# Kernel tuning notes

Measured on AMD Instinct MI355X. Metric: run time of the kernel, lower is better.

Reference implementation:

```python
import jax, jax.numpy as jnp
import numpy as np

B, XL, YL = 4, 128, 1024
D, H, L, DFF = 512, 8, 3, 2048
PV, AV, OV = 512, 1025, 1025
MASK_ID = 1024
EOS = 1024
DUR_W = 1.0
NEG = -1e9  # finite large-negative instead of -inf: keeps fully-padded rows NaN-free
HD = D // H
S = XL + 1 + YL


def sinusoid(n, d):
    pos = jnp.arange(n, dtype=jnp.float32)[:, None]
    div = jnp.exp(jnp.arange(0, d, 2, dtype=jnp.float32) * (-np.log(10000.0) / d))
    pe = jnp.zeros((n, d), dtype=jnp.float32)
    pe = pe.at[:, 0::2].set(jnp.sin(pos * div))
    pe = pe.at[:, 1::2].set(jnp.cos(pos * div))
    return pe


def layer_norm(x, g, b, eps=1e-5):
    mu = x.mean(-1, keepdims=True)
    var = ((x - mu) ** 2).mean(-1, keepdims=True)
    return (x - mu) * jax.lax.rsqrt(var + eps) * g + b


def setup_inputs():
    k = jax.random.split(jax.random.key(0), 32)
    x = jax.random.randint(k[0], (B, XL), 0, PV)
    x1_lens = jax.random.randint(k[1], (B,), 20, 60)
    x2_lens = jax.random.randint(k[2], (B,), 20, 60)
    y = jax.random.randint(k[3], (B, YL), 0, AV - 2)
    y1_lens = jax.random.randint(k[4], (B,), 100, 400)
    y2_lens = jax.random.randint(k[5], (B,), 300, 600)
    y_lens = y1_lens + 1 + y2_lens
    idx = jnp.arange(YL)[None, :]
    valid = (idx >= y1_lens[:, None] + 1) & (idx < y_lens[:, None] - 1)
    bern = jax.random.uniform(k[6], (B, YL)) < 0.3  # mask_ratio = mid(min,max)
    ym = bern & valid
    need = (~ym.any(1)) & valid.any(1)
    first = jnp.argmax(valid, axis=1)
    y_mask = ym | (need[:, None] & (idx == first[:, None]))
    emo_feature = jax.random.normal(k[7], (B, 768), dtype=jnp.float32)

    def n(kk, shape, s=0.02):
        return s * jax.random.normal(kk, shape, dtype=jnp.float32)

    inp = dict(x=x, x1_lens=x1_lens, x2_lens=x2_lens, y=y, y1_lens=y1_lens,
               y2_lens=y2_lens, y_mask=y_mask, emo_feature=emo_feature)
    inp['text_emb'] = n(k[8], (PV, D))
    inp['audio_emb'] = n(k[9], (AV, D))
    inp['type_emb'] = n(k[10], (3, D))
    inp['emo_W'] = n(k[11], (D, 768))
    inp['emo_b'] = jnp.zeros((D,), jnp.float32)
    inp['alpha_text'] = jnp.float32(1.0)
    inp['alpha_audio'] = jnp.float32(1.0)
    inp['Wqkv'] = n(k[12], (L, 3 * D, D))
    inp['bqkv'] = jnp.zeros((L, 3 * D), jnp.float32)
    inp['Wo'] = n(k[13], (L, D, D))
    inp['bo'] = jnp.zeros((L, D), jnp.float32)
    inp['ln1_g'] = jnp.ones((L, D), jnp.float32)
    inp['ln1_b'] = jnp.zeros((L, D), jnp.float32)
    inp['ln2_g'] = jnp.ones((L, D), jnp.float32)
    inp['ln2_b'] = jnp.zeros((L, D), jnp.float32)
    inp['W1'] = n(k[14], (L, DFF, D))
    inp['b1'] = jnp.zeros((L, DFF), jnp.float32)
    inp['W2'] = n(k[15], (L, D, DFF))
    inp['b2'] = jnp.zeros((L, D), jnp.float32)
    inp['predict_W'] = n(k[16], (OV, D))
    inp['dW1'] = n(k[17], (D // 2, D))
    inp['db1'] = jnp.zeros((D // 2,), jnp.float32)
    inp['dW2'] = n(k[18], (D // 4, D // 2))
    inp['db2'] = jnp.zeros((D // 4,), jnp.float32)
    inp['dW3'] = n(k[19], (1, D // 4))
    inp['db3'] = jnp.zeros((1,), jnp.float32)
    return inp


def build_attn_bias(x1_lens, x2_lens, y1_lens, y2_lens, y_mask):
    x_lens = x1_lens + 1 + x2_lens
    y_lens = y1_lens + 1 + y2_lens
    cS = jnp.arange(S)[None, :]  # [1,S] key columns
    # --- x rows ---
    rx = jnp.arange(XL)[None, :]
    is_x1 = rx < x1_lens[:, None]                                   # [B,XL]
    allow_x1 = cS < x1_lens[:, None]                                # [B,S]
    allow_x2 = (cS >= x1_lens[:, None]) & (cS < x_lens[:, None])
    x_allow = jnp.where(is_x1[:, :, None], allow_x1[:, None, :], allow_x2[:, None, :])
    # --- emo row: attends only to itself (col XL) ---
    emo_allow = jnp.broadcast_to((cS == XL)[:, None, :], (B, 1, S))
    # --- y rows ---
    ry = jnp.arange(YL)[None, :]
    is_y1 = ry < y1_lens[:, None]
    is_cls = ry == y1_lens[:, None]
    is_y2 = (ry > y1_lens[:, None]) & (ry < y_lens[:, None])
    allow_y1 = (cS < x1_lens[:, None]) | ((cS > XL) & (cS <= XL + y1_lens[:, None]))
    allow_cls = (cS < x_lens[:, None]) | (cS == XL) | ((cS > XL) & (cS <= XL + y1_lens[:, None] + 1))
    allow_y2 = (cS < x_lens[:, None]) | (cS == XL) | ((cS > XL) & (cS <= XL + y_lens[:, None]))
    ymask_full = jnp.zeros((B, S), bool).at[:, XL + 1:].set(y_mask)
    allow_y2 = allow_y2 & (~ymask_full)                             # masked tokens invisible
    y_allow = jnp.where(is_y1[:, :, None], allow_y1[:, None, :],
               jnp.where(is_cls[:, :, None], allow_cls[:, None, :],
                jnp.where(is_y2[:, :, None], allow_y2[:, None, :], False)))
    block = ~jnp.concatenate([x_allow, emo_allow, y_allow], axis=1)  # True = blocked
    return jnp.where(block, jnp.float32(NEG), jnp.float32(0.0))[:, None]  # [B,1,S,S]


def encoder_forward(h, bias, Wqkv, bqkv, Wo, bo, ln1_g, ln1_b, ln2_g, ln2_b, W1, b1, W2, b2):
    scale = 1.0 / np.sqrt(HD)
    for l in range(L):
        qkv = h @ Wqkv[l].T + bqkv[l]                               # [B,S,3D]
        q, k, v = jnp.split(qkv, 3, axis=-1)
        q = q.reshape(B, S, H, HD).transpose(0, 2, 1, 3)
        k = k.reshape(B, S, H, HD).transpose(0, 2, 1, 3)
        v = v.reshape(B, S, H, HD).transpose(0, 2, 1, 3)
        scores = jnp.einsum('bhqd,bhkd->bhqk', q, k) * scale + bias
        a = jax.nn.softmax(scores, axis=-1)
        o = jnp.einsum('bhqk,bhkd->bhqd', a, v).transpose(0, 2, 1, 3).reshape(B, S, D)
        o = o @ Wo[l].T + bo[l]
        h = layer_norm(h + o, ln1_g[l], ln1_b[l])                   # post-norm
        ff = jax.nn.relu(h @ W1[l].T + b1[l]) @ W2[l].T + b2[l]
        h = layer_norm(h + ff, ln2_g[l], ln2_b[l])
    return h


def reference(x, x1_lens, x2_lens, y, y1_lens, y2_lens, y_mask, emo_feature,
              text_emb, audio_emb, type_emb, emo_W, emo_b, alpha_text, alpha_audio,
              Wqkv, bqkv, Wo, bo, ln1_g, ln1_b, ln2_g, ln2_b, W1, b1, W2, b2,
              predict_W, dW1, db1, dW2, db2, dW3, db3):
    y_target = y
    x_emb = text_emb[x] + type_emb[0]
    x_pos = x_emb + alpha_text * sinusoid(XL, D)
    emo = emo_feature @ emo_W.T + emo_b + type_emb[1]
    y_in = jnp.where(y_mask, MASK_ID, y)
    y_emb = audio_emb[y_in] + type_emb[2]
    y_pos = y_emb + alpha_audio * sinusoid(YL, D)
    h_input = jnp.concatenate([x_pos, emo[:, None, :], y_pos], axis=1)  # [B,S,D]
    bias = build_attn_bias(x1_lens, x2_lens, y1_lens, y2_lens, y_mask)
    enc = encoder_forward(h_input, bias, Wqkv, bqkv, Wo, bo,
                          ln1_g, ln1_b, ln2_g, ln2_b, W1, b1, W2, b2)
    # duration loss on CLS hidden at prompt_lens = XL + 1 + y1_lens
    cls_hidden = enc[jnp.arange(B), XL + 1 + y1_lens]
    h1 = jax.nn.relu(cls_hidden @ dW1.T + db1)
    h2 = jax.nn.relu(h1 @ dW2.T + db2)
    pred_dur = (h2 @ dW3.T + db3)[:, 0]
    tgt_dur = y2_lens.astype(jnp.float32) / x2_lens.astype(jnp.float32)
    e = pred_dur - tgt_dur
    dur_loss = jnp.mean(jnp.where(jnp.abs(e) <= 1.0, 0.5 * e * e, jnp.abs(e) - 0.5))
    # token CE over masked positions (mean over masked tokens)
    logits = enc[:, XL + 1:] @ predict_W.T                          # [B,YL,OV]
    logp = jax.nn.log_softmax(logits, axis=-1)
    ce = -jnp.take_along_axis(logp, y_target[..., None], axis=-1)[..., 0]
    m = y_mask.astype(jnp.float32)
    token_loss = jnp.sum(ce * m) / jnp.sum(m)
    # top-3 accuracy ignoring EOS
    top3 = jax.lax.top_k(logits, 3)[1]
    correct = jnp.any(top3 == y_target[..., None], axis=-1)
    inc = (y_mask & (y_target != EOS)).astype(jnp.float32)
    acc = jnp.sum(correct.astype(jnp.float32) * inc) / jnp.maximum(jnp.sum(inc), 1.0)
    total_loss = token_loss + DUR_W * dur_loss
    return total_loss, acc
```

## Files before the change

kernel.cpp:

```cpp
#include <hip/hip_runtime.h>
#include <hip/hip_bf16.h>
#include <math.h>

#define BATCH 4
#define XL 128
#define YL 1024
#define DMODEL 512
#define NH 8
#define NLAYER 3
#define DFF 2048
#define MASK_ID 1024
#define EOS_TOK 1024
#define HD 64
#define SEQ 1153
#define OV 1025
#define NEGBIG (-1e9f)
#define QBLK 128
#define CCAP 2432

typedef unsigned short u16;
typedef short short8 __attribute__((ext_vector_type(8)));
typedef float f32x4 __attribute__((ext_vector_type(4)));

__device__ __forceinline__ u16 f2bf(float f) {
    union { float f; unsigned u; } v; v.f = f;
    unsigned r = v.u + 0x7fffu + ((v.u >> 16) & 1u);
    return (u16)(r >> 16);
}
__device__ __forceinline__ float bf2f(u16 b) {
    union { unsigned u; float f; } v; v.u = ((unsigned)b) << 16;
    return v.f;
}

__global__ __launch_bounds__(256) void cvt5_kernel(
    const float* __restrict__ s0, u16* __restrict__ d0, int n0,
    const float* __restrict__ s1, u16* __restrict__ d1, int n1,
    const float* __restrict__ s2, u16* __restrict__ d2, int n2,
    const float* __restrict__ s3, u16* __restrict__ d3, int n3,
    const float* __restrict__ s4, u16* __restrict__ d4, int n4)
{
    int c0 = n0, c1 = c0 + n1, c2 = c1 + n2, c3 = c2 + n3, c4 = c3 + n4;
    for (int i = blockIdx.x * 256 + threadIdx.x; i < c4; i += gridDim.x * 256) {
        const float* s; u16* d; int j;
        if (i < c0)      { s = s0; d = d0; j = i; }
        else if (i < c1) { s = s1; d = d1; j = i - c0; }
        else if (i < c2) { s = s2; d = d2; j = i - c1; }
        else if (i < c3) { s = s3; d = d3; j = i - c2; }
        else             { s = s4; d = d4; j = i - c3; }
        float4 v = ((const float4*)s)[j];
        ushort4 o;
        o.x = f2bf(v.x); o.y = f2bf(v.y); o.z = f2bf(v.z); o.w = f2bf(v.w);
        ((ushort4*)d)[j] = o;
    }
}

__global__ __launch_bounds__(256) void emo_kernel(
    const float* __restrict__ emo_feature, const float* __restrict__ emo_W,
    const float* __restrict__ emo_b, const float* __restrict__ type_emb,
    float* __restrict__ hbuf, u16* __restrict__ hbuf_bf)
{
    int b = blockIdx.x >> 3, c = blockIdx.x & 7;
    int t = threadIdx.x;
    int osub = t >> 2, ln = t & 3;
    int d = c * 64 + osub;
    const float* f = emo_feature + b * 768 + ln * 192;
    const float* w = emo_W + (size_t)d * 768 + ln * 192;
    float acc = 0.f;
    #pragma unroll 4
    for (int k = 0; k < 192; ++k) acc = fmaf(f[k], w[k], acc);
    acc += __shfl_xor(acc, 1);
    acc += __shfl_xor(acc, 2);
    if (ln == 0) {
        float v = acc + emo_b[d] + type_emb[DMODEL + d];
        hbuf[(size_t)(b * SEQ + XL) * DMODEL + d] = v;
        hbuf_bf[(size_t)(b * SEQ + XL) * DMODEL + d] = f2bf(v);
    }
}

__global__ __launch_bounds__(256) void build_h_kernel(
    const int* __restrict__ x, const int* __restrict__ y, const int* __restrict__ y_mask,
    const float* __restrict__ text_emb, const float* __restrict__ audio_emb,
    const float* __restrict__ type_emb,
    const float* __restrict__ alpha_text, const float* __restrict__ alpha_audio,
    float* __restrict__ hbuf, u16* __restrict__ hbuf_bf)
{
    int row = blockIdx.x * 4 + (threadIdx.x >> 6);
    int l = threadIdx.x & 63;
    int b = row / SEQ, s = row % SEQ;
    if (s == XL) return;
    int d0 = l * 8;

    const float* emb; const float* te; float alpha; int pos;
    if (s < XL) {
        int tok = x[b * XL + s];
        emb = text_emb + (size_t)tok * DMODEL;
        te = type_emb; alpha = alpha_text[0]; pos = s;
    } else {
        int r = s - XL - 1;
        int tok = y_mask[b * YL + r] ? MASK_ID : y[b * YL + r];
        emb = audio_emb + (size_t)tok * DMODEL;
        te = type_emb + 2 * DMODEL; alpha = alpha_audio[0]; pos = r;
    }

    float4 e0 = *(const float4*)(emb + d0);
    float4 e1 = *(const float4*)(emb + d0 + 4);
    float4 t0 = *(const float4*)(te + d0);
    float4 t1 = *(const float4*)(te + d0 + 4);
    float v[8] = {e0.x + t0.x, e0.y + t0.y, e0.z + t0.z, e0.w + t0.w,
                  e1.x + t1.x, e1.y + t1.y, e1.z + t1.z, e1.w + t1.w};
    float fp = (float)pos;
    #pragma unroll
    for (int p = 0; p < 4; ++p) {
        int d = d0 + 2 * p;
        float div = __expf((float)d * (-9.210340371976184f / (float)DMODEL));
        float sn, cs;
        __sincosf(fp * div, &sn, &cs);
        v[2 * p]     += alpha * sn;
        v[2 * p + 1] += alpha * cs;
    }

    float* hp = hbuf + (size_t)row * DMODEL + d0;
    *(float4*)hp       = make_float4(v[0], v[1], v[2], v[3]);
    *(float4*)(hp + 4) = make_float4(v[4], v[5], v[6], v[7]);
    short8 sv;
    #pragma unroll
    for (int e = 0; e < 8; ++e) sv[e] = (short)f2bf(v[e]);
    *(short8*)(hbuf_bf + (size_t)row * DMODEL + d0) = sv;
}

__global__ __launch_bounds__(256) void gemm_bf16_kernel(
    const u16* __restrict__ A, const u16* __restrict__ Bw,
    const float* __restrict__ bias,
    float* __restrict__ Cf, u16* __restrict__ Cb,
    int M, int N, int K, int relu)
{
    __shared__ u16 As[128 * 32];
    __shared__ u16 Bs[128 * 32];
    int tid = threadIdx.x;
    int w = tid >> 6, l = tid & 63;
    int m0 = blockIdx.y * 128, n0 = blockIdx.x * 128;
    int wm = (w >> 1) * 64, wn = (w & 1) * 64;

    f32x4 acc[4][4];
    #pragma unroll
    for (int i = 0; i < 4; ++i)
        #pragma unroll
        for (int j = 0; j < 4; ++j) acc[i][j] = (f32x4){0.f, 0.f, 0.f, 0.f};

    int srow0 = (w << 5) + (l >> 2);
    int skp = (l & 3) << 3;

    for (int k0 = 0; k0 < K; k0 += 32) {
        #pragma unroll
        for (int c = 0; c < 2; ++c) {
            int row = srow0 + c * 16;
            int am = m0 + row; if (am >= M) am = M - 1;
            int bn = n0 + row; if (bn >= N) bn = N - 1;
            __builtin_amdgcn_global_load_lds(
                (const __attribute__((address_space(1))) void*)(A + (size_t)am * K + k0 + skp),
                (__attribute__((address_space(3))) void*)(As + ((w * 2 + c) << 9)), 16, 0, 0);
            __builtin_amdgcn_global_load_lds(
                (const __attribute__((address_space(1))) void*)(Bw + (size_t)bn * K + k0 + skp),
                (__attribute__((address_space(3))) void*)(Bs + ((w * 2 + c) << 9)), 16, 0, 0);
        }
        __syncthreads();
        short8 af[4], bfr[4];
        #pragma unroll
        for (int i = 0; i < 4; ++i) {
            af[i]  = *(const short8*)(As + (wm + i * 16 + (l & 15)) * 32 + ((l >> 4) << 3));
            bfr[i] = *(const short8*)(Bs + (wn + i * 16 + (l & 15)) * 32 + ((l >> 4) << 3));
        }
        #pragma unroll
        for (int i = 0; i < 4; ++i)
            #pragma unroll
            for (int j = 0; j < 4; ++j)
                acc[i][j] = __builtin_amdgcn_mfma_f32_16x16x32_bf16(af[i], bfr[j], acc[i][j], 0, 0, 0);
        __syncthreads();
    }

    #pragma unroll
    for (int i = 0; i < 4; ++i) {
        #pragma unroll
        for (int j = 0; j < 4; ++j) {
            #pragma unroll
            for (int jj = 0; jj < 4; ++jj) {
                int row = m0 + wm + i * 16 + ((l >> 4) << 2) + jj;
                int col = n0 + wn + j * 16 + (l & 15);
                if (row < M && col < N) {
                    float v = acc[i][j][jj];
                    if (bias) v += bias[col];
                    if (relu) v = fmaxf(v, 0.f);
                    if (Cf) Cf[(size_t)row * N + col] = v;
                    if (Cb) Cb[(size_t)row * N + col] = f2bf(v);
                }
            }
        }
    }
}

__global__ __launch_bounds__(256) void gemm_bf16_splitk_kernel(
    const u16* __restrict__ A, const u16* __restrict__ Bw,
    float* __restrict__ P0, float* __restrict__ P1, float* __restrict__ P2,
    int M, int N, int K, int klen)
{
    __shared__ u16 As[128 * 32];
    __shared__ u16 Bs[128 * 32];
    int tid = threadIdx.x;
    int w = tid >> 6, l = tid & 63;
    int z = blockIdx.z;
    float* Cp = (z == 0) ? P0 : (z == 1) ? P1 : P2;
    int kbeg = z * klen;
    int kend = min(kbeg + klen, K);
    int m0 = blockIdx.y * 128, n0 = blockIdx.x * 128;
    int wm = (w >> 1) * 64, wn = (w & 1) * 64;

    f32x4 acc[4][4];
    #pragma unroll
    for (int i = 0; i < 4; ++i)
        #pragma unroll
        for (int j = 0; j < 4; ++j) acc[i][j] = (f32x4){0.f, 0.f, 0.f, 0.f};

    int srow0 = (w << 5) + (l >> 2);
    int skp = (l & 3) << 3;

    for (int k0 = kbeg; k0 < kend; k0 += 32) {
        #pragma unroll
        for (int c = 0; c < 2; ++c) {
            int row = srow0 + c * 16;
            int am = m0 + row; if (am >= M) am = M - 1;
            int bn = n0 + row; if (bn >= N) bn = N - 1;
            __builtin_amdgcn_global_load_lds(
                (const __attribute__((address_space(1))) void*)(A + (size_t)am * K + k0 + skp),
                (__attribute__((address_space(3))) void*)(As + ((w * 2 + c) << 9)), 16, 0, 0);
            __builtin_amdgcn_global_load_lds(
                (const __attribute__((address_space(1))) void*)(Bw + (size_t)bn * K + k0 + skp),
                (__attribute__((address_space(3))) void*)(Bs + ((w * 2 + c) << 9)), 16, 0, 0);
        }
        __syncthreads();
        short8 af[4], bfr[4];
        #pragma unroll
        for (int i = 0; i < 4; ++i) {
            af[i]  = *(const short8*)(As + (wm + i * 16 + (l & 15)) * 32 + ((l >> 4) << 3));
            bfr[i] = *(const short8*)(Bs + (wn + i * 16 + (l & 15)) * 32 + ((l >> 4) << 3));
        }
        #pragma unroll
        for (int i = 0; i < 4; ++i)
            #pragma unroll
            for (int j = 0; j < 4; ++j)
                acc[i][j] = __builtin_amdgcn_mfma_f32_16x16x32_bf16(af[i], bfr[j], acc[i][j], 0, 0, 0);
        __syncthreads();
    }

    #pragma unroll
    for (int i = 0; i < 4; ++i) {
        #pragma unroll
        for (int j = 0; j < 4; ++j) {
            #pragma unroll
            for (int jj = 0; jj < 4; ++jj) {
                int row = m0 + wm + i * 16 + ((l >> 4) << 2) + jj;
                int col = n0 + wn + j * 16 + (l & 15);
                if (row < M && col < N)
                    Cp[(size_t)row * N + col] = acc[i][j][jj];
            }
        }
    }
}

__global__ __launch_bounds__(256) void gemm_bf16_splitk_dynm_kernel(
    const u16* __restrict__ A, const u16* __restrict__ Bw,
    const int* __restrict__ Mp,
    float* __restrict__ P0, float* __restrict__ P1,
    int N, int K, int klen)
{
    int M = *Mp;
    int m0 = blockIdx.y * 128;
    if (m0 >= M) return;
    __shared__ u16 As[128 * 32];
    __shared__ u16 Bs[128 * 32];
    int tid = threadIdx.x;
    int w = tid >> 6, l = tid & 63;
    int z = blockIdx.z;
    float* Cp = (z == 0) ? P0 : P1;
    int kbeg = z * klen;
    int kend = min(kbeg + klen, K);
    int n0 = blockIdx.x * 128;
    int wm = (w >> 1) * 64, wn = (w & 1) * 64;

    f32x4 acc[4][4];
    #pragma unroll
    for (int i = 0; i < 4; ++i)
        #pragma unroll
        for (int j = 0; j < 4; ++j) acc[i][j] = (f32x4){0.f, 0.f, 0.f, 0.f};

    int srow0 = (w << 5) + (l >> 2);
    int skp = (l & 3) << 3;

    for (int k0 = kbeg; k0 < kend; k0 += 32) {
        #pragma unroll
        for (int c = 0; c < 2; ++c) {
            int row = srow0 + c * 16;
            int am = m0 + row; if (am >= M) am = M - 1;
            int bn = n0 + row; if (bn >= N) bn = N - 1;
            __builtin_amdgcn_global_load_lds(
                (const __attribute__((address_space(1))) void*)(A + (size_t)am * K + k0 + skp),
                (__attribute__((address_space(3))) void*)(As + ((w * 2 + c) << 9)), 16, 0, 0);
            __builtin_amdgcn_global_load_lds(
                (const __attribute__((address_space(1))) void*)(Bw + (size_t)bn * K + k0 + skp),
                (__attribute__((address_space(3))) void*)(Bs + ((w * 2 + c) << 9)), 16, 0, 0);
        }
        __syncthreads();
        short8 af[4], bfr[4];
        #pragma unroll
        for (int i = 0; i < 4; ++i) {
            af[i]  = *(const short8*)(As + (wm + i * 16 + (l & 15)) * 32 + ((l >> 4) << 3));
            bfr[i] = *(const short8*)(Bs + (wn + i * 16 + (l & 15)) * 32 + ((l >> 4) << 3));
        }
        #pragma unroll
        for (int i = 0; i < 4; ++i)
            #pragma unroll
            for (int j = 0; j < 4; ++j)
                acc[i][j] = __builtin_amdgcn_mfma_f32_16x16x32_bf16(af[i], bfr[j], acc[i][j], 0, 0, 0);
        __syncthreads();
    }

    #pragma unroll
    for (int i = 0; i < 4; ++i) {
        #pragma unroll
        for (int j = 0; j < 4; ++j) {
            #pragma unroll
            for (int jj = 0; jj < 4; ++jj) {
                int row = m0 + wm + i * 16 + ((l >> 4) << 2) + jj;
                int col = n0 + wn + j * 16 + (l & 15);
                if (row < M && col < N)
                    Cp[(size_t)row * N + col] = acc[i][j][jj];
            }
        }
    }
}

__global__ __launch_bounds__(256) void attn_mfma_kernel(
    const u16* __restrict__ qkv,
    const int* __restrict__ x1_lens, const int* __restrict__ x2_lens,
    const int* __restrict__ y1_lens, const int* __restrict__ y2_lens,
    const int* __restrict__ y_mask,
    u16* __restrict__ obuf)
{
    __shared__ u16 Ks[64 * 64];
    __shared__ u16 Vt[64 * 64];
    __shared__ u16 Ps[4][32 * 64];
    __shared__ unsigned char Am[1216];

    int tid = threadIdx.x;
    int w = tid >> 6, l = tid & 63;
    int bh = blockIdx.y;
    int b = bh >> 3, h = bh & 7;
    int q0 = blockIdx.x * QBLK;

    int x1 = x1_lens[b], xlen = x1 + 1 + x2_lens[b];
    int y1 = y1_lens[b], ylen = y1 + 1 + y2_lens[b];

    int kmax = -1;
    if (q0 < XL) kmax = max(kmax, xlen - 1);
    if (XL >= q0 && XL < q0 + QBLK) kmax = max(kmax, XL);
    {
        int ry0 = max(0, q0 - XL - 1);
        int ry1 = min(YL - 1, q0 + QBLK - 2 - XL);
        if (ry0 <= ry1) {
            if (ry0 <= y1 - 1) kmax = max(kmax, XL + y1);
            if (y1 >= ry0 && y1 <= ry1) kmax = max(kmax, XL + y1 + 1);
            int a = max(ry0, y1 + 1), bb = min(ry1, ylen - 1);
            if (a <= bb) kmax = max(kmax, XL + ylen);
        }
    }
    if (kmax < 0) return;
    int NKT = (kmax >> 6) + 1;

    for (int c = tid; c < 1216; c += 256) {
        unsigned v = 0;
        if (c < SEQ) {
            int ym = 0;
            if (c > XL) ym = y_mask[b * YL + c - XL - 1];
            bool a2c = (c == XL);
            bool ygt = (c > XL);
            bool aT0 = (c < x1);
            bool aT1 = (c >= x1) && (c < xlen);
            bool aT3 = aT0 || (ygt && c <= XL + y1);
            bool aT4 = (c < xlen) || a2c || (ygt && c <= XL + y1 + 1);
            bool aT5 = (((c < xlen) || a2c || (ygt && c <= XL + ylen)) && !ym);
            v = (aT0 ? 1u : 0u) | (aT1 ? 2u : 0u) | (a2c ? 4u : 0u) |
                (aT3 ? 8u : 0u) | (aT4 ? 16u : 0u) | (aT5 ? 32u : 0u);
        }
        Am[c] = (unsigned char)v;
    }

    short8 qf[2][2];
    #pragma unroll
    for (int qh = 0; qh < 2; ++qh) {
        int qr = q0 + w * 32 + qh * 16 + (l & 15);
        const u16* qp = qkv + (size_t)(b * SEQ + qr) * 1536 + h * 64 + ((l >> 4) << 3);
        #pragma unroll
        for (int kb = 0; kb < 2; ++kb) {
            short8 raw = *(const short8*)(qp + kb * 32);
            short8 s8;
            #pragma unroll
            for (int e = 0; e < 8; ++e)
                s8[e] = (short)f2bf(bf2f((u16)raw[e]) * 0.125f);
            qf[qh][kb] = s8;
        }
    }

    int rt[2][4];
    #pragma unroll
    for (int qh = 0; qh < 2; ++qh)
        #pragma unroll
        for (int j = 0; j < 4; ++j) {
            int qrj = q0 + w * 32 + qh * 16 + ((l >> 4) << 2) + j;
            int t;
            if (qrj < XL) t = (qrj < x1) ? 0 : 1;
            else if (qrj == XL) t = 2;
            else {
                int ry = qrj - XL - 1;
                t = (ry < y1) ? 3 : (ry == y1) ? 4 : (ry < ylen) ? 5 : 7;
            }
            rt[qh][j] = t;
        }

    f32x4 oacc[2][4];
    #pragma unroll
    for (int qh = 0; qh < 2; ++qh)
        #pragma unroll
        for (int db = 0; db < 4; ++db) oacc[qh][db] = (f32x4){0.f, 0.f, 0.f, 0.f};
    float mrun[2][4], lrun[2][4];
    #pragma unroll
    for (int qh = 0; qh < 2; ++qh)
        #pragma unroll
        for (int j = 0; j < 4; ++j) { mrun[qh][j] = -INFINITY; lrun[qh][j] = 0.f; }
    u16* Psw = &Ps[w][0];

    for (int kt = 0; kt < NKT; ++kt) {
        __syncthreads();
        {
            int r = tid >> 2, d0k = (tid & 3) << 4;
            int krc = min(kt * 64 + r, SEQ - 1);
            const u16* kp = qkv + (size_t)(b * SEQ + krc) * 1536 + 512 + h * 64 + d0k;
            short8 ka = *(const short8*)kp;
            short8 kb8 = *(const short8*)(kp + 8);
            int ksw = (r & 7) << 3;
            *(short8*)&Ks[r * 64 + (d0k ^ ksw)] = ka;
            *(short8*)&Ks[r * 64 + ((d0k + 8) ^ ksw)] = kb8;
        }
        {
            int rp = tid >> 3, o = tid & 7;
            int d0v = o * 8;
            int k0r = min(kt * 64 + 2 * rp, SEQ - 1);
            int k1r = min(kt * 64 + 2 * rp + 1, SEQ - 1);
            const u16* v0p = qkv + (size_t)(b * SEQ + k0r) * 1536 + 1024 + h * 64 + d0v;
            const u16* v1p = qkv + (size_t)(b * SEQ + k1r) * 1536 + 1024 + h * 64 + d0v;
            short8 va = *(const short8*)v0p;
            short8 vb = *(const short8*)v1p;
            #pragma unroll
            for (int e = 0; e < 8; ++e) {
                int d = d0v + e;
                unsigned val = (unsigned)(u16)va[e] | ((unsigned)(u16)vb[e] << 16);
                *(unsigned*)&Vt[d * 64 + ((2 * rp) ^ ((d & 7) << 3))] = val;
            }
        }
        __syncthreads();

        unsigned amv[4];
        #pragma unroll
        for (int cb = 0; cb < 4; ++cb)
            amv[cb] = Am[kt * 64 + cb * 16 + (l & 15)];

        f32x4 sc[2][4];
        #pragma unroll
        for (int cb = 0; cb < 4; ++cb) {
            int krw = cb * 16 + (l & 15);
            int ksw = (krw & 7) << 3;
            short8 k0 = *(const short8*)&Ks[krw * 64 + ((((l >> 4) << 3)) ^ ksw)];
            short8 k1 = *(const short8*)&Ks[krw * 64 + ((32 + ((l >> 4) << 3)) ^ ksw)];
            #pragma unroll
            for (int qh = 0; qh < 2; ++qh) {
                f32x4 z = (f32x4){0.f, 0.f, 0.f, 0.f};
                z = __builtin_amdgcn_mfma_f32_16x16x32_bf16(qf[qh][0], k0, z, 0, 0, 0);
                sc[qh][cb] = __builtin_amdgcn_mfma_f32_16x16x32_bf16(qf[qh][1], k1, z, 0, 0, 0);
            }
        }

        #pragma unroll
        for (int qh = 0; qh < 2; ++qh) {
            #pragma unroll
            for (int j = 0; j < 4; ++j) {
                int rtj = rt[qh][j];
                float s0 = ((amv[0] >> rtj) & 1u) ? sc[qh][0][j] : NEGBIG;
                float s1 = ((amv[1] >> rtj) & 1u) ? sc[qh][1][j] : NEGBIG;
                float s2 = ((amv[2] >> rtj) & 1u) ? sc[qh][2][j] : NEGBIG;
                float s3 = ((amv[3] >> rtj) & 1u) ? sc[qh][3][j] : NEGBIG;
                float tmax = fmaxf(fmaxf(s0, s1), fmaxf(s2, s3));
                tmax = fmaxf(tmax, __shfl_xor(tmax, 1));
                tmax = fmaxf(tmax, __shfl_xor(tmax, 2));
                tmax = fmaxf(tmax, __shfl_xor(tmax, 4));
                tmax = fmaxf(tmax, __shfl_xor(tmax, 8));
                float newm = fmaxf(mrun[qh][j], tmax);
                float corr = __expf(mrun[qh][j] - newm);
                float p0 = __expf(s0 - newm);
                float p1 = __expf(s1 - newm);
                float p2 = __expf(s2 - newm);
                float p3 = __expf(s3 - newm);
                float ps = p0 + p1 + p2 + p3;
                ps += __shfl_xor(ps, 1); ps += __shfl_xor(ps, 2);
                ps += __shfl_xor(ps, 4); ps += __shfl_xor(ps, 8);
                lrun[qh][j] = lrun[qh][j] * corr + ps;
                mrun[qh][j] = newm;
                #pragma unroll
                for (int db = 0; db < 4; ++db) oacc[qh][db][j] *= corr;
                int lr = qh * 16 + ((l >> 4) << 2) + j;
                int sw = (lr & 7) << 3;
                Psw[lr * 64 + ((0  + (l & 15)) ^ sw)] = f2bf(p0);
                Psw[lr * 64 + ((16 + (l & 15)) ^ sw)] = f2bf(p1);
                Psw[lr * 64 + ((32 + (l & 15)) ^ sw)] = f2bf(p2);
                Psw[lr * 64 + ((48 + (l & 15)) ^ sw)] = f2bf(p3);
            }
        }

        short8 pf[2][2];
        #pragma unroll
        for (int qh = 0; qh < 2; ++qh) {
            int pr = qh * 16 + (l & 15);
            int sw = (pr & 7) << 3;
            pf[qh][0] = *(const short8*)&Psw[pr * 64 + ((((l >> 4) << 3)) ^ sw)];
            pf[qh][1] = *(const short8*)&Psw[pr * 64 + ((32 + ((l >> 4) << 3)) ^ sw)];
        }
        #pragma unroll
        for (int db = 0; db < 4; ++db) {
            int vr = db * 16 + (l & 15);
            int vsw = (vr & 7) << 3;
            short8 v0 = *(const short8*)&Vt[vr * 64 + ((((l >> 4) << 3)) ^ vsw)];
            short8 v1 = *(const short8*)&Vt[vr * 64 + ((32 + ((l >> 4) << 3)) ^ vsw)];
            #pragma unroll
            for (int qh = 0; qh < 2; ++qh) {
                oacc[qh][db] = __builtin_amdgcn_mfma_f32_16x16x32_bf16(pf[qh][0], v0, oacc[qh][db], 0, 0, 0);
                oacc[qh][db] = __builtin_amdgcn_mfma_f32_16x16x32_bf16(pf[qh][1], v1, oacc[qh][db], 0, 0, 0);
            }
        }
    }

    #pragma unroll
    for (int qh = 0; qh < 2; ++qh) {
        float rl[4];
        #pragma unroll
        for (int j = 0; j < 4; ++j) rl[j] = 1.f / lrun[qh][j];
        #pragma unroll
        for (int db = 0; db < 4; ++db) {
            #pragma unroll
            for (int j = 0; j < 4; ++j) {
                int qrj = q0 + w * 32 + qh * 16 + ((l >> 4) << 2) + j;
                obuf[(size_t)(b * SEQ + qrj) * DMODEL + h * 64 + db * 16 + (l & 15)] =
                    f2bf(oacc[qh][db][j] * rl[j]);
            }
        }
    }
}

__global__ __launch_bounds__(256) void add_ln_kernel(
    float* __restrict__ hbuf, u16* __restrict__ hbuf_bf,
    const float* __restrict__ p0, const float* __restrict__ p1,
    const float* __restrict__ p2, const float* __restrict__ bias,
    const float* __restrict__ g, const float* __restrict__ beta)
{
    int row = blockIdx.x * 4 + (threadIdx.x >> 6);
    int l = threadIdx.x & 63;
    int d0 = l * 8;
    size_t off = (size_t)row * DMODEL + d0;
    float* hp = hbuf + off;
    float4 a0 = *(const float4*)hp, a1 = *(const float4*)(hp + 4);
    float4 q0 = *(const float4*)(p0 + off), q1 = *(const float4*)(p0 + off + 4);
    float v[8] = {a0.x + q0.x, a0.y + q0.y, a0.z + q0.z, a0.w + q0.w,
                  a1.x + q1.x, a1.y + q1.y, a1.z + q1.z, a1.w + q1.w};
    if (p1) {
        float4 r0 = *(const float4*)(p1 + off), r1 = *(const float4*)(p1 + off + 4);
        v[0] += r0.x; v[1] += r0.y; v[2] += r0.z; v[3] += r0.w;
        v[4] += r1.x; v[5] += r1.y; v[6] += r1.z; v[7] += r1.w;
    }
    if (p2) {
        float4 r0 = *(const float4*)(p2 + off), r1 = *(const float4*)(p2 + off + 4);
        v[0] += r0.x; v[1] += r0.y; v[2] += r0.z; v[3] += r0.w;
        v[4] += r1.x; v[5] += r1.y; v[6] += r1.z; v[7] += r1.w;
    }
    {
        float4 b0 = *(const float4*)(bias + d0), b1 = *(const float4*)(bias + d0 + 4);
        v[0] += b0.x; v[1] += b0.y; v[2] += b0.z; v[3] += b0.w;
        v[4] += b1.x; v[5] += b1.y; v[6] += b1.z; v[7] += b1.w;
    }
    float s = 0.f;
    #pragma unroll
    for (int e = 0; e < 8; ++e) s += v[e];
    #pragma unroll
    for (int off2 = 32; off2 > 0; off2 >>= 1) s += __shfl_xor(s, off2);
    float mu = s * (1.f / DMODEL);
    float sq = 0.f;
    #pragma unroll
    for (int e = 0; e < 8; ++e) { v[e] -= mu; sq += v[e] * v[e]; }
    #pragma unroll
    for (int off2 = 32; off2 > 0; off2 >>= 1) sq += __shfl_xor(sq, off2);
    float inv = 1.f / sqrtf(sq * (1.f / DMODEL) + 1e-5f);
    float4 g0 = *(const float4*)(g + d0), g1 = *(const float4*)(g + d0 + 4);
    float4 be0 = *(const float4*)(beta + d0), be1 = *(const float4*)(beta + d0 + 4);
    float o[8];
    o[0] = v[0] * inv * g0.x + be0.x; o[1] = v[1] * inv * g0.y + be0.y;
    o[2] = v[2] * inv * g0.z + be0.z; o[3] = v[3] * inv * g0.w + be0.w;
    o[4] = v[4] * inv * g1.x + be1.x; o[5] = v[5] * inv * g1.y + be1.y;
    o[6] = v[6] * inv * g1.z + be1.z; o[7] = v[7] * inv * g1.w + be1.w;
    *(float4*)hp       = make_float4(o[0], o[1], o[2], o[3]);
    *(float4*)(hp + 4) = make_float4(o[4], o[5], o[6], o[7]);
    short8 sv;
    #pragma unroll
    for (int e = 0; e < 8; ++e) sv[e] = (short)f2bf(o[e]);
    *(short8*)(hbuf_bf + off) = sv;
}

__global__ __launch_bounds__(256) void init_accum_kernel(float* accum) {
    if (threadIdx.x < 8) accum[threadIdx.x] = 0.f;
}

__global__ __launch_bounds__(256) void compact_kernel(
    const int* __restrict__ y_mask, int* __restrict__ cnt, int* __restrict__ cmap)
{
    int i = blockIdx.x * 256 + threadIdx.x;
    if (i < BATCH * YL && y_mask[i]) {
        int pos = atomicAdd(cnt, 1);
        cmap[pos] = i;
    }
}

__global__ __launch_bounds__(256) void copy_rows_kernel(
    const int* __restrict__ cnt, const int* __restrict__ cmap,
    const u16* __restrict__ hbuf_bf, const int* __restrict__ y,
    u16* __restrict__ cbuf, int* __restrict__ ctgt)
{
    int i = blockIdx.x;
    if (i >= *cnt) return;
    int g = cmap[i];
    int b = g >> 10, r = g & 1023;
    const u16* src = hbuf_bf + (size_t)(b * SEQ + XL + 1 + r) * DMODEL;
    u16* dst = cbuf + (size_t)i * DMODEL;
    int t = threadIdx.x;
    ((ushort2*)dst)[t] = ((const ushort2*)src)[t];
    if (t == 0) ctgt[i] = y[g];
}

__global__ __launch_bounds__(256) void ce_kernel(
    const int* __restrict__ cnt,
    const float* __restrict__ lg0, const float* __restrict__ lg1,
    const int* __restrict__ ctgt, float* __restrict__ accum)
{
    int row = blockIdx.x;
    if (row >= *cnt) return;
    const float* lp0 = lg0 + (size_t)row * OV;
    const float* lp1 = lg1 + (size_t)row * OV;
    int tgt = ctgt[row];
    int t = threadIdx.x;
    __shared__ float red[4];

    float lmax = -INFINITY;
    for (int i = t; i < OV; i += 256) lmax = fmaxf(lmax, lp0[i] + lp1[i]);
    #pragma unroll
    for (int off = 32; off > 0; off >>= 1) lmax = fmaxf(lmax, __shfl_xor(lmax, off));
    if ((t & 63) == 0) red[t >> 6] = lmax;
    __syncthreads();
    lmax = fmaxf(fmaxf(red[0], red[1]), fmaxf(red[2], red[3]));
    __syncthreads();

    float lsum = 0.f;
    for (int i = t; i < OV; i += 256) lsum += expf(lp0[i] + lp1[i] - lmax);
    #pragma unroll
    for (int off = 32; off > 0; off >>= 1) lsum += __shfl_xor(lsum, off);
    if ((t & 63) == 0) red[t >> 6] = lsum;
    __syncthreads();
    lsum = red[0] + red[1] + red[2] + red[3];
    __syncthreads();

    float lt = lp0[tgt] + lp1[tgt];
    float cntr = 0.f;
    for (int i = t; i < OV; i += 256) {
        float v = lp0[i] + lp1[i];
        if (v > lt || (v == lt && i < tgt)) cntr += 1.f;
    }
    #pragma unroll
    for (int off = 32; off > 0; off >>= 1) cntr += __shfl_xor(cntr, off);
    if ((t & 63) == 0) red[t >> 6] = cntr;
    __syncthreads();
    cntr = red[0] + red[1] + red[2] + red[3];

    if (t == 0) {
        float ce = -(lt - lmax - logf(lsum));
        float inc = (tgt != EOS_TOK) ? 1.f : 0.f;
        float corr = (cntr < 2.5f) ? 1.f : 0.f;
        atomicAdd(&accum[0], ce);
        atomicAdd(&accum[1], 1.f);
        atomicAdd(&accum[2], corr * inc);
        atomicAdd(&accum[3], inc);
    }
}

__global__ __launch_bounds__(256) void dur1_kernel(
    const float* __restrict__ hbuf, const int* __restrict__ y1_lens,
    const float* __restrict__ dW1, const float* __restrict__ db1,
    float* __restrict__ h1buf)
{
    __shared__ float cls[DMODEL];
    int g = blockIdx.x;
    int b = g >> 3, c = g & 7;
    int t = threadIdx.x;
    const float* cp = hbuf + (size_t)(b * SEQ + XL + 1 + y1_lens[b]) * DMODEL;
    cls[t] = cp[t]; cls[t + 256] = cp[t + 256];
    __syncthreads();
    int row = c * 32 + (t >> 3);
    int ln = t & 7;
    const float* w = dW1 + (size_t)row * DMODEL + ln * 64;
    const float* cv = cls + ln * 64;
    float acc = 0.f;
    #pragma unroll 8
    for (int k = 0; k < 64; ++k) acc = fmaf(cv[k], w[k], acc);
    acc += __shfl_xor(acc, 1); acc += __shfl_xor(acc, 2); acc += __shfl_xor(acc, 4);
    if (ln == 0) h1buf[b * 256 + row] = fmaxf(acc + db1[row], 0.f);
}

__global__ __launch_bounds__(256) void dur2_kernel(
    const float* __restrict__ h1buf,
    const float* __restrict__ dW2, const float* __restrict__ db2,
    const float* __restrict__ dW3, const float* __restrict__ db3,
    float* __restrict__ preds)
{
    __shared__ float h1s[256];
    __shared__ float h2s[128];
    int b = blockIdx.x;
    int t = threadIdx.x;
    h1s[t] = h1buf[b * 256 + t];
    __syncthreads();
    if (t < 128) {
        float acc = db2[t];
        const float* w = dW2 + (size_t)t * 256;
        for (int k = 0; k < 256; ++k) acc = fmaf(h1s[k], w[k], acc);
        h2s[t] = fmaxf(acc, 0.f);
    }
    __syncthreads();
    if (t < 64) {
        float v = h2s[t] * dW3[t] + h2s[t + 64] * dW3[t + 64];
        #pragma unroll
        for (int off = 32; off > 0; off >>= 1) v += __shfl_xor(v, off);
        if (t == 0) preds[b] = v + db3[0];
    }
}

__global__ __launch_bounds__(64) void final_kernel(
    const float* __restrict__ accum, const float* __restrict__ preds,
    const int* __restrict__ y2_lens, const int* __restrict__ x2_lens,
    float* __restrict__ out)
{
    if (threadIdx.x == 0) {
        float dl = 0.f;
        for (int b = 0; b < BATCH; ++b) {
            float tgt = (float)y2_lens[b] / (float)x2_lens[b];
            float e = preds[b] - tgt;
            float ae = fabsf(e);
            dl += (ae <= 1.f) ? 0.5f * e * e : (ae - 0.5f);
        }
        dl *= (1.f / BATCH);
        float token_loss = accum[0] / accum[1];
        float acc_v = accum[2] / fmaxf(accum[3], 1.f);
        out[0] = token_loss + dl;
        out[1] = acc_v;
    }
}

extern "C" void kernel_launch(void* const* d_in, const int* in_sizes, int n_in,
                              void* d_out, int out_size, void* d_ws, size_t ws_size,
                              hipStream_t stream)
{
    const int*   x           = (const int*)d_in[0];
    const int*   x1_lens     = (const int*)d_in[1];
    const int*   x2_lens     = (const int*)d_in[2];
    const int*   y           = (const int*)d_in[3];
    const int*   y1_lens     = (const int*)d_in[4];
    const int*   y2_lens     = (const int*)d_in[5];
    const int*   y_mask      = (const int*)d_in[6];
    const float* emo_feature = (const float*)d_in[7];
    const float* text_emb    = (const float*)d_in[8];
    const float* audio_emb   = (const float*)d_in[9];
    const float* type_emb    = (const float*)d_in[10];
    const float* emo_W       = (const float*)d_in[11];
    const float* emo_b       = (const float*)d_in[12];
    const float* alpha_text  = (const float*)d_in[13];
    const float* alpha_audio = (const float*)d_in[14];
    const float* Wqkv        = (const float*)d_in[15];
    const float* bqkv        = (const float*)d_in[16];
    const float* Wo          = (const float*)d_in[17];
    const float* bo          = (const float*)d_in[18];
    const float* ln1_g       = (const float*)d_in[19];
    const float* ln1_b       = (const float*)d_in[20];
    const float* ln2_g       = (const float*)d_in[21];
    const float* ln2_b       = (const float*)d_in[22];
    const float* W1          = (const float*)d_in[23];
    const float* b1          = (const float*)d_in[24];
    const float* W2          = (const float*)d_in[25];
    const float* b2          = (const float*)d_in[26];
    const float* predict_W   = (const float*)d_in[27];
    const float* dW1         = (const float*)d_in[28];
    const float* db1         = (const float*)d_in[29];
    const float* dW2         = (const float*)d_in[30];
    const float* db2         = (const float*)d_in[31];
    const float* dW3         = (const float*)d_in[32];
    const float* db3         = (const float*)d_in[33];

    const int M = BATCH * SEQ;
    char* p = (char*)d_ws;
    float* hbuf   = (float*)p; p += 9445376;
    float* delta  = (float*)p; p += 9445376;
    char*  uni    = p;         p += 18909440;
    u16*   hbuf_bf = (u16*)p;  p += 4722688;
    u16*   qkv_bf  = (u16*)p;  p += 14168064;
    u16*   obuf_bf = (u16*)p;  p += 4722688;
    u16*   wbf     = (u16*)p;  p += 19923968;
    u16*   cbuf    = (u16*)p;  p += (size_t)CCAP * DMODEL * 2;
    u16*   ff1_bf  = (u16*)uni;

    float* partA = (float*)qkv_bf;
    float* partB = (float*)((char*)qkv_bf + 9445376);
    float* lg0   = (float*)uni;
    float* lg1   = (float*)qkv_bf;

    float* accum  = delta;
    int*   cnt    = (int*)(delta + 4);
    float* preds  = delta + 8;
    int*   cmap   = (int*)(delta + 16);
    int*   ctgt   = cmap + CCAP;
    float* h1buf  = (float*)(ctgt + CCAP);

    u16* wq_bf = wbf;
    u16* wo_bf = wq_bf + 2359296;
    u16* w1_bf = wo_bf + 786432;
    u16* w2_bf = w1_bf + 3145728;
    u16* wp_bf = w2_bf + 3145728;

    cvt5_kernel<<<1024, 256, 0, stream>>>(
        Wqkv, wq_bf, 2359296 / 4,
        Wo, wo_bf, 786432 / 4,
        W1, w1_bf, 3145728 / 4,
        W2, w2_bf, 3145728 / 4,
        predict_W, wp_bf, 524800 / 4);

    emo_kernel<<<32, 256, 0, stream>>>(emo_feature, emo_W, emo_b, type_emb, hbuf, hbuf_bf);
    build_h_kernel<<<M / 4, 256, 0, stream>>>(
        x, y, y_mask, text_emb, audio_emb, type_emb,
        alpha_text, alpha_audio, hbuf, hbuf_bf);

    const int MG = (M + 127) / 128;
    for (int l = 0; l < NLAYER; ++l) {
        gemm_bf16_kernel<<<dim3(12, MG), 256, 0, stream>>>(
            hbuf_bf, wq_bf + (size_t)l * 1536 * 512, bqkv + l * 1536,
            nullptr, qkv_bf, M, 1536, 512, 0);
        attn_mfma_kernel<<<dim3((SEQ + QBLK - 1) / QBLK, BATCH * NH), 256, 0, stream>>>(
            qkv_bf, x1_lens, x2_lens, y1_lens, y2_lens, y_mask, obuf_bf);
        gemm_bf16_splitk_kernel<<<dim3(4, MG, 2), 256, 0, stream>>>(
            obuf_bf, wo_bf + (size_t)l * 512 * 512,
            delta, partA, nullptr, M, 512, 512, 256);
        add_ln_kernel<<<M / 4, 256, 0, stream>>>(hbuf, hbuf_bf,
            delta, partA, nullptr, bo + l * 512,
            ln1_g + l * DMODEL, ln1_b + l * DMODEL);
        gemm_bf16_kernel<<<dim3(16, MG), 256, 0, stream>>>(
            hbuf_bf, w1_bf + (size_t)l * 2048 * 512, b1 + l * 2048,
            nullptr, ff1_bf, M, 2048, 512, 1);
        gemm_bf16_splitk_kernel<<<dim3(4, MG, 3), 256, 0, stream>>>(
            ff1_bf, w2_bf + (size_t)l * 512 * 2048,
            delta, partA, partB, M, 512, 2048, 768);
        add_ln_kernel<<<M / 4, 256, 0, stream>>>(hbuf, hbuf_bf,
            delta, partA, partB, b2 + l * 512,
            ln2_g + l * DMODEL, ln2_b + l * DMODEL);
    }

    init_accum_kernel<<<1, 64, 0, stream>>>(accum);
    compact_kernel<<<(BATCH * YL) / 256, 256, 0, stream>>>(y_mask, cnt, cmap);
    copy_rows_kernel<<<CCAP, 256, 0, stream>>>(cnt, cmap, hbuf_bf, y, cbuf, ctgt);
    gemm_bf16_splitk_dynm_kernel<<<dim3((OV + 127) / 128, CCAP / 128, 2), 256, 0, stream>>>(
        cbuf, wp_bf, cnt, lg0, lg1, OV, 512, 256);
    ce_kernel<<<CCAP, 256, 0, stream>>>(cnt, lg0, lg1, ctgt, accum);

    dur1_kernel<<<32, 256, 0, stream>>>(hbuf, y1_lens, dW1, db1, h1buf);
    dur2_kernel<<<4, 256, 0, stream>>>(h1buf, dW2, db2, dW3, db3, preds);
    final_kernel<<<1, 64, 0, stream>>>(accum, preds, y2_lens, x2_lens, (float*)d_out);
}
```

Before: 610.8 us.

## Restructure attention: transposed S=K·Q^T, register-shuffled P, bitmask masks, 512 threads

Rewrites the attention kernel so 8 waves each own 16 query rows instead of 4 waves owning 32. Scores are computed as K·Q^T, which puts each query's scores across lanes and makes the softmax reductions cheaper. P is rearranged into MFMA operand layout with register shuffles rather than a round trip through shared memory. The per-column mask byte array is replaced by ballot-built 64-bit masks per row type and key tile. The aim is to cut LDS traffic and shuffle-heavy reductions and to raise parallelism per block, at the cost of more cross-lane shuffles and half the work per wave.

After: 598.2 us. 1.02x faster.

```diff
diff --git a/kernel.cpp b/kernel.cpp
--- a/kernel.cpp
+++ b/kernel.cpp
@@ -19,6 +19,7 @@
 #define CCAP 2432
 
 typedef unsigned short u16;
+typedef unsigned int u32;
 typedef short short8 __attribute__((ext_vector_type(8)));
 typedef float f32x4 __attribute__((ext_vector_type(4)));
 
@@ -338,7 +339,7 @@
     }
 }
 
-__global__ __launch_bounds__(256) void attn_mfma_kernel(
+__global__ __launch_bounds__(512) void attn_mfma_kernel(
     const u16* __restrict__ qkv,
     const int* __restrict__ x1_lens, const int* __restrict__ x2_lens,
     const int* __restrict__ y1_lens, const int* __restrict__ y2_lens,
@@ -347,11 +348,11 @@
 {
     __shared__ u16 Ks[64 * 64];
     __shared__ u16 Vt[64 * 64];
-    __shared__ u16 Ps[4][32 * 64];
-    __shared__ unsigned char Am[1216];
+    __shared__ unsigned long long Bits[7][19];
 
     int tid = threadIdx.x;
     int w = tid >> 6, l = tid & 63;
+    int g = l >> 4;
     int bh = blockIdx.y;
     int b = bh >> 3, h = bh & 7;
     int q0 = blockIdx.x * QBLK;
@@ -375,189 +376,183 @@
     if (kmax < 0) return;
     int NKT = (kmax >> 6) + 1;
 
-    for (int c = tid; c < 1216; c += 256) {
-        unsigned v = 0;
-        if (c < SEQ) {
-            int ym = 0;
-            if (c > XL) ym = y_mask[b * YL + c - XL - 1];
-            bool a2c = (c == XL);
-            bool ygt = (c > XL);
-            bool aT0 = (c < x1);
-            bool aT1 = (c >= x1) && (c < xlen);
-            bool aT3 = aT0 || (ygt && c <= XL + y1);
-            bool aT4 = (c < xlen) || a2c || (ygt && c <= XL + y1 + 1);
-            bool aT5 = (((c < xlen) || a2c || (ygt && c <= XL + ylen)) && !ym);
-            v = (aT0 ? 1u : 0u) | (aT1 ? 2u : 0u) | (a2c ? 4u : 0u) |
-                (aT3 ? 8u : 0u) | (aT4 ? 16u : 0u) | (aT5 ? 32u : 0u);
-        }
-        Am[c] = (unsigned char)v;
-    }
-
-    short8 qf[2][2];
-    #pragma unroll
-    for (int qh = 0; qh < 2; ++qh) {
-        int qr = q0 + w * 32 + qh * 16 + (l & 15);
-        const u16* qp = qkv + (size_t)(b * SEQ + qr) * 1536 + h * 64 + ((l >> 4) << 3);
-        #pragma unroll
-        for (int kb = 0; kb < 2; ++kb) {
-            short8 raw = *(const short8*)(qp + kb * 32);
-            short8 s8;
-            #pragma unroll
-            for (int e = 0; e < 8; ++e)
-                s8[e] = (short)f2bf(bf2f((u16)raw[e]) * 0.125f);
-            qf[qh][kb] = s8;
-        }
-    }
-
-    int rt[2][4];
-    #pragma unroll
-    for (int qh = 0; qh < 2; ++qh)
-        #pragma unroll
-        for (int j = 0; j < 4; ++j) {
-            int qrj = q0 + w * 32 + qh * 16 + ((l >> 4) << 2) + j;
-            int t;
-            if (qrj < XL) t = (qrj < x1) ? 0 : 1;
-            else if (qrj == XL) t = 2;
+    for (int pp = w; pp < 7 * 19; pp += 8) {
+        int ty = pp / 19, tile = pp - ty * 19;
+        int c = tile * 64 + l;
+        bool allow = false;
+        if (c < SEQ && ty < 6) {
+            bool a2c = (c == XL), ygt = (c > XL);
+            if (ty == 0) allow = (c < x1);
+            else if (ty == 1) allow = (c >= x1) && (c < xlen);
+            else if (ty == 2) allow = a2c;
+            else if (ty == 3) allow = (c < x1) || (ygt && c <= XL + y1);
+            else if (ty == 4) allow = (c < xlen) || a2c || (ygt && c <= XL + y1 + 1);
             else {
-                int ry = qrj - XL - 1;
-                t = (ry < y1) ? 3 : (ry == y1) ? 4 : (ry < ylen) ? 5 : 7;
+                int ym = ygt ? y_mask[b * YL + c - XL - 1] : 0;
+                allow = (((c < xlen) || a2c || (ygt && c <= XL + ylen)) && !ym);
             }
-            rt[qh][j] = t;
-        }
-
-    f32x4 oacc[2][4];
-    #pragma unroll
-    for (int qh = 0; qh < 2; ++qh)
-        #pragma unroll
-        for (int db = 0; db < 4; ++db) oacc[qh][db] = (f32x4){0.f, 0.f, 0.f, 0.f};
-    float mrun[2][4], lrun[2][4];
-    #pragma unroll
-    for (int qh = 0; qh < 2; ++qh)
-        #pragma unroll
-        for (int j = 0; j < 4; ++j) { mrun[qh][j] = -INFINITY; lrun[qh][j] = 0.f; }
-    u16* Psw = &Ps[w][0];
+        }
+        unsigned long long mk = __ballot(allow);
+        if (l == 0) Bits[ty][tile] = mk;
+    }
+
+    int qr = q0 + w * 16 + (l & 15);
+    int qrc = min(qr, SEQ - 1);
+    short8 qf0, qf1;
+    {
+        const u16* qp = qkv + (size_t)(b * SEQ + qrc) * 1536 + h * 64 + (g << 3);
+        short8 r0 = *(const short8*)qp;
+        short8 r1 = *(const short8*)(qp + 32);
+        #pragma unroll
+        for (int e = 0; e < 8; ++e) {
+            qf0[e] = (short)f2bf(bf2f((u16)r0[e]) * 0.125f);
+            qf1[e] = (short)f2bf(bf2f((u16)r1[e]) * 0.125f);
+        }
+    }
+
+    int rt;
+    {
+        if (qr >= SEQ) rt = 6;
+        else if (qr < XL) rt = (qr < x1) ? 0 : 1;
+        else if (qr == XL) rt = 2;
+        else {
+            int ry = qr - XL - 1;
+            rt = (ry < y1) ? 3 : (ry == y1) ? 4 : (ry < ylen) ? 5 : 6;
+        }
+    }
+
+    f32x4 oacc[4];
+    #pragma unroll
+    for (int db = 0; db < 4; ++db) oacc[db] = (f32x4){0.f, 0.f, 0.f, 0.f};
+    float mrun = -INFINITY, lrun = 0.f;
+
+    int srcA = (l & 15) + ((g & 1) << 5);
+    int srcB = srcA + 16;
+    bool hi = (g >> 1) & 1;
 
     for (int kt = 0; kt < NKT; ++kt) {
         __syncthreads();
         {
-            int r = tid >> 2, d0k = (tid & 3) << 4;
+            int r = tid >> 3, d0k = (tid & 7) << 3;
             int krc = min(kt * 64 + r, SEQ - 1);
-            const u16* kp = qkv + (size_t)(b * SEQ + krc) * 1536 + 512 + h * 64 + d0k;
-            short8 ka = *(const short8*)kp;
-            short8 kb8 = *(const short8*)(kp + 8);
-            int ksw = (r & 7) << 3;
-            *(short8*)&Ks[r * 64 + (d0k ^ ksw)] = ka;
-            *(short8*)&Ks[r * 64 + ((d0k + 8) ^ ksw)] = kb8;
+            short8 ka = *(const short8*)(qkv + (size_t)(b * SEQ + krc) * 1536 + 512 + h * 64 + d0k);
+            *(short8*)&Ks[r * 64 + (d0k ^ ((r & 7) << 3))] = ka;
         }
         {
-            int rp = tid >> 3, o = tid & 7;
-            int d0v = o * 8;
+            int rp = tid >> 4, o = tid & 15;
+            int d0v = o * 4;
             int k0r = min(kt * 64 + 2 * rp, SEQ - 1);
             int k1r = min(kt * 64 + 2 * rp + 1, SEQ - 1);
-            const u16* v0p = qkv + (size_t)(b * SEQ + k0r) * 1536 + 1024 + h * 64 + d0v;
-            const u16* v1p = qkv + (size_t)(b * SEQ + k1r) * 1536 + 1024 + h * 64 + d0v;
-            short8 va = *(const short8*)v0p;
-            short8 vb = *(const short8*)v1p;
-            #pragma unroll
-            for (int e = 0; e < 8; ++e) {
+            ushort4 va = *(const ushort4*)(qkv + (size_t)(b * SEQ + k0r) * 1536 + 1024 + h * 64 + d0v);
+            ushort4 vb = *(const ushort4*)(qkv + (size_t)(b * SEQ + k1r) * 1536 + 1024 + h * 64 + d0v);
+            u32 pv[4] = {(u32)va.x | ((u32)vb.x << 16), (u32)va.y | ((u32)vb.y << 16),
+                         (u32)va.z | ((u32)vb.z << 16), (u32)va.w | ((u32)vb.w << 16)};
+            #pragma unroll
+            for (int e = 0; e < 4; ++e) {
                 int d = d0v + e;
-                unsigned val = (unsigned)(u16)va[e] | ((unsigned)(u16)vb[e] << 16);
-                *(unsigned*)&Vt[d * 64 + ((2 * rp) ^ ((d & 7) << 3))] = val;
+                *(u32*)&Vt[d * 64 + ((2 * rp) ^ ((d & 7) << 3))] = pv[e];
             }
         }
         __syncthreads();
 
-        unsigned amv[4];
-        #pragma unroll
-        for (int cb = 0; cb < 4; ++cb)
-            amv[cb] = Am[kt * 64 + cb * 16 + (l & 15)];
-
-        f32x4 sc[2][4];
+        f32x4 sc[4];
         #pragma unroll
         for (int cb = 0; cb < 4; ++cb) {
             int krw = cb * 16 + (l & 15);
             int ksw = (krw & 7) << 3;
-            short8 k0 = *(const short8*)&Ks[krw * 64 + ((((l >> 4) << 3)) ^ ksw)];
-            short8 k1 = *(const short8*)&Ks[krw * 64 + ((32 + ((l >> 4) << 3)) ^ ksw)];
-            #pragma unroll
-            for (int qh = 0; qh < 2; ++qh) {
-                f32x4 z = (f32x4){0.f, 0.f, 0.f, 0.f};
-                z = __builtin_amdgcn_mfma_f32_16x16x32_bf16(qf[qh][0], k0, z, 0, 0, 0);
-                sc[qh][cb] = __builtin_amdgcn_mfma_f32_16x16x32_bf16(qf[qh][1], k1, z, 0, 0, 0);
+            short8 k0 = *(const short8*)&Ks[krw * 64 + ((g << 3) ^ ksw)];
+            short8 k1 = *(const short8*)&Ks[krw * 64 + ((32 + (g << 3)) ^ ksw)];
+            f32x4 z = (f32x4){0.f, 0.f, 0.f, 0.f};
+            z = __builtin_amdgcn_mfma_f32_16x16x32_bf16(k0, qf0, z, 0, 0, 0);
+            sc[cb] = __builtin_amdgcn_mfma_f32_16x16x32_bf16(k1, qf1, z, 0, 0, 0);
+        }
+
+        unsigned long long mb = Bits[rt][kt];
+        #pragma unroll
+        for (int cb = 0; cb < 4; ++cb) {
+            unsigned nib = (unsigned)(mb >> (16 * cb + 4 * g)) & 0xFu;
+            #pragma unroll
+            for (int r = 0; r < 4; ++r)
+                sc[cb][r] = ((nib >> r) & 1u) ? sc[cb][r] : NEGBIG;
+        }
+
+        float tmax = sc[0][0];
+        #pragma unroll
+        for (int cb = 0; cb < 4; ++cb)
+            #pragma unroll
+            for (int r = 0; r < 4; ++r) tmax = fmaxf(tmax, sc[cb][r]);
+        tmax = fmaxf(tmax, __shfl_xor(tmax, 16));
+        tmax = fmaxf(tmax, __shfl_xor(tmax, 32));
+        float newm = fmaxf(mrun, tmax);
+        float corr = __expf(mrun - newm);
+        float p[4][4];
+        float ps = 0.f;
+        #pragma unroll
+        for (int cb = 0; cb < 4; ++cb)
+            #pragma unroll
+            for (int r = 0; r < 4; ++r) {
+                p[cb][r] = __expf(sc[cb][r] - newm);
+                ps += p[cb][r];
             }
-        }
-
-        #pragma unroll
-        for (int qh = 0; qh < 2; ++qh) {
-            #pragma unroll
-            for (int j = 0; j < 4; ++j) {
-                int rtj = rt[qh][j];
-                float s0 = ((amv[0] >> rtj) & 1u) ? sc[qh][0][j] : NEGBIG;
-                float s1 = ((amv[1] >> rtj) & 1u) ? sc[qh][1][j] : NEGBIG;
-                float s2 = ((amv[2] >> rtj) & 1u) ? sc[qh][2][j] : NEGBIG;
-                float s3 = ((amv[3] >> rtj) & 1u) ? sc[qh][3][j] : NEGBIG;
-                float tmax = fmaxf(fmaxf(s0, s1), fmaxf(s2, s3));
-                tmax = fmaxf(tmax, __shfl_xor(tmax, 1));
-                tmax = fmaxf(tmax, __shfl_xor(tmax, 2));
-                tmax = fmaxf(tmax, __shfl_xor(tmax, 4));
-                tmax = fmaxf(tmax, __shfl_xor(tmax, 8));
-                float newm = fmaxf(mrun[qh][j], tmax);
-                float corr = __expf(mrun[qh][j] - newm);
-                float p0 = __expf(s0 - newm);
-                float p1 = __expf(s1 - newm);
-                float p2 = __expf(s2 - newm);
-                float p3 = __expf(s3 - newm);
-                float ps = p0 + p1 + p2 + p3;
-                ps += __shfl_xor(ps, 1); ps += __shfl_xor(ps, 2);
-                ps += __shfl_xor(ps, 4); ps += __shfl_xor(ps, 8);
-                lrun[qh][j] = lrun[qh][j] * corr + ps;
-                mrun[qh][j] = newm;
-                #pragma unroll
-                for (int db = 0; db < 4; ++db) oacc[qh][db][j] *= corr;
-                int lr = qh * 16 + ((l >> 4) << 2) + j;
-                int sw = (lr & 7) << 3;
-                Psw[lr * 64 + ((0  + (l & 15)) ^ sw)] = f2bf(p0);
-                Psw[lr * 64 + ((16 + (l & 15)) ^ sw)] = f2bf(p1);
-                Psw[lr * 64 + ((32 + (l & 15)) ^ sw)] = f2bf(p2);
-                Psw[lr * 64 + ((48 + (l & 15)) ^ sw)] = f2bf(p3);
-            }
-        }
-
-        short8 pf[2][2];
-        #pragma unroll
-        for (int qh = 0; qh < 2; ++qh) {
-            int pr = qh * 16 + (l & 15);
-            int sw = (pr & 7) << 3;
-            pf[qh][0] = *(const short8*)&Psw[pr * 64 + ((((l >> 4) << 3)) ^ sw)];
-            pf[qh][1] = *(const short8*)&Psw[pr * 64 + ((32 + ((l >> 4) << 3)) ^ sw)];
-        }
+        ps += __shfl_xor(ps, 16);
+        ps += __shfl_xor(ps, 32);
+        lrun = lrun * corr + ps;
+        mrun = newm;
+
+        float cr[4];
+        #pragma unroll
+        for (int r = 0; r < 4; ++r) cr[r] = __shfl(corr, (g << 2) + r);
+        #pragma unroll
+        for (int db = 0; db < 4; ++db)
+            #pragma unroll
+            for (int r = 0; r < 4; ++r) oacc[db][r] *= cr[r];
+
+        u32 P0[4], P1[4];
+        #pragma unroll
+        for (int cb = 0; cb < 4; ++cb) {
+            P0[cb] = (u32)f2bf(p[cb][0]) | ((u32)f2bf(p[cb][1]) << 16);
+            P1[cb] = (u32)f2bf(p[cb][2]) | ((u32)f2bf(p[cb][3]) << 16);
+        }
+
+        union { u32 u[4]; short8 s; } f1, f2;
+        {
+            u32 a0 = __shfl(P0[0], srcA), a1 = __shfl(P1[0], srcA);
+            u32 a2 = __shfl(P0[0], srcB), a3 = __shfl(P1[0], srcB);
+            u32 b0 = __shfl(P0[1], srcA), b1 = __shfl(P1[1], srcA);
+            u32 b2 = __shfl(P0[1], srcB), b3 = __shfl(P1[1], srcB);
+            f1.u[0] = hi ? b0 : a0; f1.u[1] = hi ? b1 : a1;
+            f1.u[2] = hi ? b2 : a2; f1.u[3] = hi ? b3 : a3;
+            u32 c0 = __shfl(P0[2], srcA), c1 = __shfl(P1[2], srcA);
+            u32 c2 = __shfl(P0[2], srcB), c3 = __shfl(P1[2], srcB);
+            u32 d0 = __shfl(P0[3], srcA), d1 = __shfl(P1[3], srcA);
+            u32 d2 = __shfl(P0[3], srcB), d3 = __shfl(P1[3], srcB);
+            f2.u[0] = hi ? d0 : c0; f2.u[1] = hi ? d1 : c1;
+            f2.u[2] = hi ? d2 : c2; f2.u[3] = hi ? d3 : c3;
+        }
+
         #pragma unroll
         for (int db = 0; db < 4; ++db) {
             int vr = db * 16 + (l & 15);
             int vsw = (vr & 7) << 3;
-            short8 v0 = *(const short8*)&Vt[vr * 64 + ((((l >> 4) << 3)) ^ vsw)];
-            short8 v1 = *(const short8*)&Vt[vr * 64 + ((32 + ((l >> 4) << 3)) ^ vsw)];
-            #pragma unroll
-            for (int qh = 0; qh < 2; ++qh) {
-                oacc[qh][db] = __builtin_amdgcn_mfma_f32_16x16x32_bf16(pf[qh][0], v0, oacc[qh][db], 0, 0, 0);
-                oacc[qh][db] = __builtin_amdgcn_mfma_f32_16x16x32_bf16(pf[qh][1], v1, oacc[qh][db], 0, 0, 0);
-            }
-        }
-    }
-
-    #pragma unroll
-    for (int qh = 0; qh < 2; ++qh) {
-        float rl[4];
-        #pragma unroll
-        for (int j = 0; j < 4; ++j) rl[j] = 1.f / lrun[qh][j];
-        #pragma unroll
-        for (int db = 0; db < 4; ++db) {
-            #pragma unroll
-            for (int j = 0; j < 4; ++j) {
-                int qrj = q0 + w * 32 + qh * 16 + ((l >> 4) << 2) + j;
+            short8 v0 = *(const short8*)&Vt[vr * 64 + ((g << 3) ^ vsw)];
+            short8 v1 = *(const short8*)&Vt[vr * 64 + ((32 + (g << 3)) ^ vsw)];
+            oacc[db] = __builtin_amdgcn_mfma_f32_16x16x32_bf16(f1.s, v0, oacc[db], 0, 0, 0);
+            oacc[db] = __builtin_amdgcn_mfma_f32_16x16x32_bf16(f2.s, v1, oacc[db], 0, 0, 0);
+        }
+    }
+
+    float rinv = 1.f / lrun;
+    float rl[4];
+    #pragma unroll
+    for (int r = 0; r < 4; ++r) rl[r] = __shfl(rinv, (g << 2) + r);
+    #pragma unroll
+    for (int db = 0; db < 4; ++db) {
+        #pragma unroll
+        for (int r = 0; r < 4; ++r) {
+            int qrj = q0 + w * 16 + (g << 2) + r;
+            if (qrj < SEQ)
                 obuf[(size_t)(b * SEQ + qrj) * DMODEL + h * 64 + db * 16 + (l & 15)] =
-                    f2bf(oacc[qh][db][j] * rl[j]);
-            }
+                    f2bf(oacc[db][r] * rl[r]);
         }
     }
 }
@@ -860,7 +855,7 @@
         gemm_bf16_kernel<<<dim3(12, MG), 256, 0, stream>>>(
             hbuf_bf, wq_bf + (size_t)l * 1536 * 512, bqkv + l * 1536,
             nullptr, qkv_bf, M, 1536, 512, 0);
-        attn_mfma_kernel<<<dim3((SEQ + QBLK - 1) / QBLK, BATCH * NH), 256, 0, stream>>>(
+        attn_mfma_kernel<<<dim3((SEQ + QBLK - 1) / QBLK, BATCH * NH), 512, 0, stream>>>(
             qkv_bf, x1_lens, x2_lens, y1_lens, y2_lens, y_mask, obuf_bf);
         gemm_bf16_splitk_kernel<<<dim3(4, MG, 2), 256, 0, stream>>>(
             obuf_bf, wo_bf + (size_t)l * 512 * 512,
```
